# Optimization experiments

Hardware: AMD Instinct MI355X
Metric: run time of the kernel (lower is better)

Reference implementation:

```python
import jax, jax.numpy as jnp
import numpy as np

N_NODES = 50000
HIDDEN = 128
N_EDGES = 800000


def gcn_conv(x, edge_index, W, b):
    # PyG GCNConv: h = x @ W (no bias); add self-loops; symmetric norm; scatter-add; + bias
    h = x @ W  # [N, H]
    row, col = edge_index[0], edge_index[1]
    sl = jnp.arange(N_NODES)
    row_f = jnp.concatenate([row, sl])
    col_f = jnp.concatenate([col, sl])
    ones = jnp.ones(row_f.shape[0], dtype=x.dtype)
    deg = jax.ops.segment_sum(ones, col_f, num_segments=N_NODES)  # in-degree incl self-loop
    dinv = jnp.where(deg > 0, jax.lax.rsqrt(deg), 0.0)
    norm = dinv[row_f] * dinv[col_f]  # [E+N]
    msgs = h[row_f] * norm[:, None]   # gather + scale
    out = jax.ops.segment_sum(msgs, col_f, num_segments=N_NODES)  # scatter-add
    return out + b


def setup_inputs() -> dict:
    key = jax.random.key(0)
    ks = jax.random.split(key, 12)
    H = HIDDEN
    s = 1.0 / np.sqrt(H)
    x = jax.random.normal(ks[0], (N_NODES, H), dtype=jnp.float32)
    edge_index = jax.random.randint(ks[1], (2, N_EDGES), 0, N_NODES, dtype=jnp.int64)
    W1 = jax.random.uniform(ks[2], (H, H), jnp.float32, -s, s)
    b1 = jax.random.uniform(ks[3], (H,), jnp.float32, -s, s)
    W2 = jax.random.uniform(ks[4], (H, H), jnp.float32, -s, s)
    b2 = jax.random.uniform(ks[5], (H,), jnp.float32, -s, s)
    s2 = 1.0 / np.sqrt(2 * H)
    We1 = jax.random.uniform(ks[6], (2 * H, H), jnp.float32, -s2, s2)
    be1 = jax.random.uniform(ks[7], (H,), jnp.float32, -s2, s2)
    We2 = jax.random.uniform(ks[8], (H, 1), jnp.float32, -s, s)
    be2 = jax.random.uniform(ks[9], (1,), jnp.float32, -s, s)
    return {"x": x, "edge_index": edge_index, "W1": W1, "b1": b1, "W2": W2,
            "b2": b2, "We1": We1, "be1": be1, "We2": We2, "be2": be2}


def reference(x, edge_index, W1, b1, W2, b2, We1, be1, We2, be2):
    h = jax.nn.relu(gcn_conv(x, edge_index, W1, b1))
    h = jax.nn.relu(gcn_conv(h, edge_index, W2, b2))
    row, col = edge_index[0], edge_index[1]
    ef = jnp.concatenate([h[row], h[col]], axis=1)  # [E, 2H]
    z = jax.nn.relu(ef @ We1 + be1)
    p = jax.nn.sigmoid(z @ We2 + be2)  # [E, 1]
    return p.squeeze(-1)
```

## Files before the change

### kernel.cpp

```cpp
#include <hip/hip_runtime.h>
#include <math.h>

#define NND 50000
#define HD  128
#define NE  800000
#define NBK 196
#define BINB 391
#define NCH 391

typedef unsigned short u16;
typedef unsigned int   u32;
typedef __attribute__((ext_vector_type(8))) short bf16x8;
typedef __attribute__((ext_vector_type(4))) float f32x4;

__device__ __forceinline__ float bf2f(u32 u) {
  union { u32 i; float f; } v; v.i = u << 16; return v.f;
}
__device__ __forceinline__ u16 f2bf(float f) {
  union { float f; u32 i; } v; v.f = f;
  return (u16)((v.i + 0x7FFFu + ((v.i >> 16) & 1u)) >> 16);
}
__device__ __forceinline__ void unpack8(uint4 m, float* f) {
  f[0] = bf2f(m.x & 0xFFFFu); f[1] = bf2f(m.x >> 16);
  f[2] = bf2f(m.y & 0xFFFFu); f[3] = bf2f(m.y >> 16);
  f[4] = bf2f(m.z & 0xFFFFu); f[5] = bf2f(m.z >> 16);
  f[6] = bf2f(m.w & 0xFFFFu); f[7] = bf2f(m.w >> 16);
}

__global__ __launch_bounds__(256) void k_prep(const int* __restrict__ col, u32* __restrict__ bhist,
                                              const float* __restrict__ W1, const float* __restrict__ W2,
                                              const float* __restrict__ We1,
                                              u16* __restrict__ t1h, u16* __restrict__ t1l,
                                              u16* __restrict__ t2h, u16* __restrict__ t2l,
                                              u16* __restrict__ teh, u16* __restrict__ tel) {
  __shared__ u32 lh[NBK];
  int tid = threadIdx.x;
  if (blockIdx.x < BINB) {
    if (tid < NBK) lh[tid] = 0;
    __syncthreads();
    int e0 = blockIdx.x * 2048;
    #pragma unroll
    for (int s = 0; s < 8; ++s) {
      int e = e0 + s * 256 + tid;
      if (e < NE) atomicAdd(&lh[col[e] >> 8], 1u);
    }
    __syncthreads();
    if (tid < NBK && lh[tid]) atomicAdd(&bhist[tid], lh[tid]);
    return;
  }
  int idx = (blockIdx.x - BINB) * 256 + tid;
  float w;
  u16 *dh, *dl;
  int j;
  if (idx < 16384) {
    j = idx; int n = j >> 7, k = j & 127;
    w = W1[k * 128 + n]; dh = t1h; dl = t1l;
  } else if (idx < 32768) {
    j = idx - 16384; int n = j >> 7, k = j & 127;
    w = W2[k * 128 + n]; dh = t2h; dl = t2l;
  } else {
    j = idx - 32768; int n = j >> 7, k = j & 127;
    w = (n < 128) ? We1[k * 128 + n] : We1[(128 + k) * 128 + (n - 128)];
    dh = teh; dl = tel;
  }
  int n = j >> 7, k = j & 127;
  int sidx = n * 128 + ((((k >> 3) ^ (n & 7))) << 3) + (k & 7);
  u16 hi = f2bf(w);
  float res = w - bf2f((u32)hi);
  dh[sidx] = hi;
  dl[sidx] = f2bf(res);
}

__global__ __launch_bounds__(256) void k_bscan(const u32* __restrict__ bhist, u32* __restrict__ bbase,
                                               u32* __restrict__ bcur) {
  __shared__ u32 ws[4];
  int tid = threadIdx.x, lane = tid & 63, wid = tid >> 6;
  u32 d = (tid < NBK) ? bhist[tid] : 0;
  u32 x = d;
  #pragma unroll
  for (int off = 1; off < 64; off <<= 1) {
    u32 y = __shfl_up(x, off);
    if (lane >= off) x += y;
  }
  if (lane == 63) ws[wid] = x;
  __syncthreads();
  u32 woff = 0;
  for (int w = 0; w < wid; ++w) woff += ws[w];
  if (tid < NBK) { bbase[tid] = woff + x - d; bcur[tid] = woff + x - d; }
}

__global__ __launch_bounds__(256) void k_bin(const int* __restrict__ row, const int* __restrict__ col,
                                             u32* __restrict__ bcur, uint2* __restrict__ recs) {
  __shared__ u32 lcount[NBK], lbase[NBK];
  int tid = threadIdx.x;
  if (tid < NBK) lcount[tid] = 0;
  __syncthreads();
  int e0 = blockIdx.x * 2048;
  u32 rank[8]; int cv[8];
  #pragma unroll
  for (int s = 0; s < 8; ++s) {
    int e = e0 + s * 256 + tid;
    if (e < NE) {
      cv[s] = col[e];
      rank[s] = atomicAdd(&lcount[cv[s] >> 8], 1u);
    }
  }
  __syncthreads();
  if (tid < NBK && lcount[tid]) lbase[tid] = atomicAdd(&bcur[tid], lcount[tid]);
  __syncthreads();
  #pragma unroll
  for (int s = 0; s < 8; ++s) {
    int e = e0 + s * 256 + tid;
    if (e < NE) {
      int c = cv[s];
      u32 slot = lbase[c >> 8] + rank[s];
      recs[slot] = make_uint2((u32)row[e] | (((u32)c & 255u) << 16), (u32)e);
    }
  }
}

__global__ __launch_bounds__(256) void k_fine(const u32* __restrict__ bhist, const u32* __restrict__ bbase,
                                              const uint2* __restrict__ recs, uint2* __restrict__ sre,
                                              int* __restrict__ ptr, float* __restrict__ dinv) {
  __shared__ u32 lh[256];
  __shared__ u32 ws[4];
  int b = blockIdx.x, tid = threadIdx.x, lane = tid & 63, wid = tid >> 6;
  u32 base = bbase[b], cnt = bhist[b];
  lh[tid] = 0;
  __syncthreads();
  for (u32 i = tid; i < cnt; i += 256) atomicAdd(&lh[(recs[base + i].x >> 16) & 255u], 1u);
  __syncthreads();
  u32 ci = lh[tid];
  u32 x = ci;
  #pragma unroll
  for (int off = 1; off < 64; off <<= 1) {
    u32 y = __shfl_up(x, off);
    if (lane >= off) x += y;
  }
  if (lane == 63) ws[wid] = x;
  __syncthreads();
  u32 woff = 0;
  for (int w = 0; w < wid; ++w) woff += ws[w];
  u32 excl = woff + x - ci;
  int node = b * 256 + tid;
  if (node <= NND) ptr[node] = (int)(base + excl);
  if (node < NND) dinv[node] = rsqrtf((float)(ci + 1));
  __syncthreads();
  lh[tid] = excl;
  __syncthreads();
  for (u32 i = tid; i < cnt; i += 256) {
    uint2 rec = recs[base + i];
    u32 r = atomicAdd(&lh[(rec.x >> 16) & 255u], 1u);
    sre[base + r] = make_uint2(rec.x & 0xFFFFu, rec.y);
  }
}

__device__ __forceinline__ void mm_body(const void* Xv, bool afp32,
                                        const u16* Whi, const u16* Wlo,
                                        u16* OUT, const float* scale, int ostride,
                                        const float* bias) {
  __shared__ __align__(16) u16 Bh[128 * 128];
  __shared__ __align__(16) u16 Bl[128 * 128];
  int tid = threadIdx.x;
  int h = blockIdx.x / NCH;
  int chunk = blockIdx.x - h * NCH;
  Whi += (size_t)h * 128 * 128;
  Wlo += (size_t)h * 128 * 128;
  int ooff = h * 128;
  {
    const uint4* gh = (const uint4*)Whi;
    const uint4* gl = (const uint4*)Wlo;
    uint4* lh = (uint4*)Bh;
    uint4* ll = (uint4*)Bl;
    #pragma unroll
    for (int i = 0; i < 4; ++i) {
      lh[tid + i * 512] = gh[tid + i * 512];
      ll[tid + i * 512] = gl[tid + i * 512];
    }
  }
  __syncthreads();
  int wid = tid >> 6, lane = tid & 63;
  int m16 = lane & 15, kg = lane >> 4;
  int arow = chunk * 128 + wid * 16 + m16;
  int ar = (arow < NND) ? arow : NND - 1;
  bf16x8 afrag[4];
  if (afp32) {
    const float* X = (const float*)Xv + (size_t)ar * 128 + kg * 8;
    #pragma unroll
    for (int ks = 0; ks < 4; ++ks) {
      float4 a = *(const float4*)(X + ks * 32);
      float4 b = *(const float4*)(X + ks * 32 + 4);
      union { u32 w[4]; bf16x8 v; } u;
      u.w[0] = (u32)f2bf(a.x) | ((u32)f2bf(a.y) << 16);
      u.w[1] = (u32)f2bf(a.z) | ((u32)f2bf(a.w) << 16);
      u.w[2] = (u32)f2bf(b.x) | ((u32)f2bf(b.y) << 16);
      u.w[3] = (u32)f2bf(b.z) | ((u32)f2bf(b.w) << 16);
      afrag[ks] = u.v;
    }
  } else {
    const u16* X = (const u16*)Xv + (size_t)ar * 128 + kg * 8;
    #pragma unroll
    for (int ks = 0; ks < 4; ++ks) afrag[ks] = *(const bf16x8*)(X + ks * 32);
  }
  int crow0 = chunk * 128 + wid * 16 + kg * 4;
  float sc[4];
  #pragma unroll
  for (int j = 0; j < 4; ++j)
    sc[j] = (scale != nullptr && crow0 + j < NND) ? scale[crow0 + j] : 1.0f;
  #pragma unroll
  for (int t = 0; t < 8; ++t) {
    int coln = t * 16 + m16;
    float badd = (bias != nullptr && h != 0) ? bias[coln] : 0.f;
    f32x4 acc = {0.f, 0.f, 0.f, 0.f};
    #pragma unroll
    for (int ks = 0; ks < 4; ++ks) {
      int c8 = (ks * 4 + kg) ^ (coln & 7);
      bf16x8 bhf = *(const bf16x8*)(Bh + coln * 128 + c8 * 8);
      bf16x8 blf = *(const bf16x8*)(Bl + coln * 128 + c8 * 8);
      acc = __builtin_amdgcn_mfma_f32_16x16x32_bf16(afrag[ks], bhf, acc, 0, 0, 0);
      acc = __builtin_amdgcn_mfma_f32_16x16x32_bf16(afrag[ks], blf, acc, 0, 0, 0);
    }
    #pragma unroll
    for (int j = 0; j < 4; ++j) {
      int r = crow0 + j;
      if (r < NND) OUT[(size_t)r * ostride + ooff + coln] = f2bf(acc[j] * sc[j] + badd);
    }
  }
}

template<bool AFP32>
__global__ __launch_bounds__(512) void k_mm(const void* __restrict__ Xv,
                                            const u16* __restrict__ Whi, const u16* __restrict__ Wlo,
                                            u16* __restrict__ OUT, const float* __restrict__ scale,
                                            int ostride, const float* __restrict__ bias) {
  mm_body(Xv, AFP32, Whi, Wlo, OUT, scale, ostride, bias);
}

__global__ __launch_bounds__(256) void k_gather(const int* __restrict__ ptr, const uint2* __restrict__ sre,
                                                const float* __restrict__ dinv, const u16* __restrict__ Ts,
                                                u16* __restrict__ H, const float* __restrict__ bias) {
  int wid = threadIdx.x >> 6, lane = threadIdx.x & 63;
  int ch8 = lane & 15, slot = lane >> 4;
  int v = blockIdx.x * 4 + wid; if (v >= NND) return;
  int p0 = ptr[v], p1 = ptr[v + 1];
  const uint4* T4 = (const uint4*)Ts;
  float acc[8];
  if (slot == 0) {
    uint4 m = T4[(size_t)v * 16 + ch8];
    unpack8(m, acc);
  } else {
    #pragma unroll
    for (int k = 0; k < 8; ++k) acc[k] = 0.f;
  }
  for (int j2 = p0; j2 < p1; j2 += 32) {
    bool ok[8]; int r[8];
    #pragma unroll
    for (int u = 0; u < 8; ++u) {
      int j = j2 + u * 4 + slot;
      ok[u] = j < p1;
      r[u] = (int)sre[ok[u] ? j : p0].x;
    }
    uint4 m[8];
    #pragma unroll
    for (int u = 0; u < 8; ++u) m[u] = T4[(size_t)r[u] * 16 + ch8];
    #pragma unroll
    for (int u = 0; u < 8; ++u) {
      if (ok[u]) {
        float f[8]; unpack8(m[u], f);
        #pragma unroll
        for (int k = 0; k < 8; ++k) acc[k] += f[k];
      }
    }
  }
  #pragma unroll
  for (int k = 0; k < 8; ++k) {
    acc[k] += __shfl_xor(acc[k], 16);
    acc[k] += __shfl_xor(acc[k], 32);
  }
  if (slot == 0) {
    float s = dinv[v];
    float4 ba = *(const float4*)(bias + ch8 * 8);
    float4 bb = *(const float4*)(bias + ch8 * 8 + 4);
    float bv[8] = {ba.x, ba.y, ba.z, ba.w, bb.x, bb.y, bb.z, bb.w};
    u32 pk[4];
    #pragma unroll
    for (int k = 0; k < 4; ++k) {
      float o0 = fmaxf(fmaf(acc[2 * k], s, bv[2 * k]), 0.f);
      float o1 = fmaxf(fmaf(acc[2 * k + 1], s, bv[2 * k + 1]), 0.f);
      pk[k] = (u32)f2bf(o0) | ((u32)f2bf(o1) << 16);
    }
    *(uint4*)(H + (size_t)v * 128 + ch8 * 8) = make_uint4(pk[0], pk[1], pk[2], pk[3]);
  }
}

__global__ __launch_bounds__(256) void k_edge(const int* __restrict__ ptr, const uint2* __restrict__ sre,
                                              const u16* __restrict__ UV,
                                              const float* __restrict__ We2,
                                              const float* __restrict__ be2, float* __restrict__ out) {
  int wid = threadIdx.x >> 6, lane = threadIdx.x & 63;
  int ch8 = lane & 15, slot = lane >> 4;
  int c = blockIdx.x * 4 + wid; if (c >= NND) return;
  int p0 = ptr[c], p1 = ptr[c + 1];
  if (p0 == p1) return;
  const uint4* UV4 = (const uint4*)UV;
  float vv[8];
  {
    uint4 mv = UV4[(size_t)c * 32 + 16 + ch8];
    unpack8(mv, vv);
  }
  float w2[8];
  {
    float4 wa = *(const float4*)(We2 + ch8 * 8);
    float4 wb = *(const float4*)(We2 + ch8 * 8 + 4);
    w2[0] = wa.x; w2[1] = wa.y; w2[2] = wa.z; w2[3] = wa.w;
    w2[4] = wb.x; w2[5] = wb.y; w2[6] = wb.z; w2[7] = wb.w;
  }
  float bias2 = be2[0];
  for (int j2 = p0; j2 < p1; j2 += 32) {
    bool ok[8]; uint2 e[8];
    #pragma unroll
    for (int u = 0; u < 8; ++u) {
      int j = j2 + u * 4 + slot;
      ok[u] = j < p1;
      e[u] = sre[ok[u] ? j : p0];
    }
    uint4 m[8];
    #pragma unroll
    for (int u = 0; u < 8; ++u) m[u] = UV4[(size_t)e[u].x * 32 + ch8];
    float p[8];
    #pragma unroll
    for (int u = 0; u < 8; ++u) {
      float f[8]; unpack8(m[u], f);
      float s0 = fmaxf(f[0] + vv[0], 0.f) * w2[0] + fmaxf(f[1] + vv[1], 0.f) * w2[1];
      s0 += fmaxf(f[2] + vv[2], 0.f) * w2[2] + fmaxf(f[3] + vv[3], 0.f) * w2[3];
      s0 += fmaxf(f[4] + vv[4], 0.f) * w2[4] + fmaxf(f[5] + vv[5], 0.f) * w2[5];
      s0 += fmaxf(f[6] + vv[6], 0.f) * w2[6] + fmaxf(f[7] + vv[7], 0.f) * w2[7];
      p[u] = s0;
    }
    #pragma unroll
    for (int off = 8; off; off >>= 1) {
      #pragma unroll
      for (int u = 0; u < 8; ++u) p[u] += __shfl_xor(p[u], off);
    }
    if (ch8 == 0) {
      #pragma unroll
      for (int u = 0; u < 8; ++u)
        if (ok[u]) out[e[u].y] = 1.f / (1.f + __expf(-(p[u] + bias2)));
    }
  }
}

extern "C" void kernel_launch(void* const* d_in, const int* in_sizes, int n_in,
                              void* d_out, int out_size, void* d_ws, size_t ws_size,
                              hipStream_t stream) {
  const float* x   = (const float*)d_in[0];
  const int*   ei  = (const int*)d_in[1];
  const float* W1  = (const float*)d_in[2];
  const float* b1  = (const float*)d_in[3];
  const float* W2  = (const float*)d_in[4];
  const float* b2  = (const float*)d_in[5];
  const float* We1 = (const float*)d_in[6];
  const float* be1 = (const float*)d_in[7];
  const float* We2 = (const float*)d_in[8];
  const float* be2 = (const float*)d_in[9];
  float* out = (float*)d_out;

  const int* row  = ei;
  const int* colp = ei + NE;

  if (ws_size < (size_t)16166240 * 4) return;
  int*   ptr    = (int*)d_ws;
  float* dinv   = (float*)d_ws + 50064;
  u32*   bhist  = (u32*)d_ws + 100112;
  u32*   bbase  = (u32*)d_ws + 100308;
  u32*   bcur   = (u32*)d_ws + 100504;
  uint2* recs   = (uint2*)((u32*)d_ws + 100704);
  uint2* sre    = (uint2*)((u32*)d_ws + 1700704);
  u16*   t1h    = (u16*)((u32*)d_ws + 3300704);
  u16*   t1l    = (u16*)((u32*)d_ws + 3308896);
  u16*   t2h    = (u16*)((u32*)d_ws + 3317088);
  u16*   t2l    = (u16*)((u32*)d_ws + 3325280);
  u16*   teh    = (u16*)((u32*)d_ws + 3333472);
  u16*   tel    = (u16*)((u32*)d_ws + 3349856);
  u16*   Ts     = (u16*)((u32*)d_ws + 3366240);
  u16*   H      = (u16*)((u32*)d_ws + 6566240);
  u16*   UV     = (u16*)((u32*)d_ws + 9766240);

  (void)hipMemsetAsync(bhist, 0, NBK * sizeof(u32), stream);
  k_prep <<<BINB + 256, 256, 0, stream>>>(colp, bhist, W1, W2, We1, t1h, t1l, t2h, t2l, teh, tel);
  k_bscan<<<1, 256, 0, stream>>>(bhist, bbase, bcur);
  k_bin  <<<BINB, 256, 0, stream>>>(row, colp, bcur, recs);
  k_fine <<<NBK, 256, 0, stream>>>(bhist, bbase, recs, sre, ptr, dinv);

  int node_grid = (NND + 3) / 4;

  k_mm<true><<<NCH, 512, 0, stream>>>(x, t1h, t1l, Ts, dinv, 128, nullptr);
  k_gather<<<node_grid, 256, 0, stream>>>(ptr, sre, dinv, Ts, H, b1);

  k_mm<false><<<NCH, 512, 0, stream>>>(H, t2h, t2l, Ts, dinv, 128, nullptr);
  k_gather<<<node_grid, 256, 0, stream>>>(ptr, sre, dinv, Ts, H, b2);

  k_mm<false><<<2 * NCH, 512, 0, stream>>>(H, teh, tel, UV, nullptr, 256, be1);
  k_edge<<<node_grid, 256, 0, stream>>>(ptr, sre, UV, We2, be2, out);
}
```

Before: 206.0 us.

## Re-sort edges by source range and make edge scoring edge-parallel

Adds a stable counting sort (histogram, scan, place) that groups the column-sorted edge list into 8 buckets by source-node range, and packs the destination node into the upper bits of each record. The final edge kernel now gives each wave a fixed run of 32 edges instead of one destination node. It reloads the destination's V vector only when the destination changes, and gathers U rows from a narrower source range so they are more likely to stay in cache. This removes per-node load imbalance and improves gather locality, at the cost of three extra small kernels and another edge-array pass.

```diff
diff --git a/kernel.cpp b/kernel.cpp
--- a/kernel.cpp
+++ b/kernel.cpp
@@ -7,9 +7,13 @@
 #define NBK 196
 #define BINB 391
 #define NCH 391
+#define RB  8
+#define RBSZ 6250
+#define RBLK 391
 
 typedef unsigned short u16;
 typedef unsigned int   u32;
+typedef unsigned long long u64;
 typedef __attribute__((ext_vector_type(8))) short bf16x8;
 typedef __attribute__((ext_vector_type(4))) float f32x4;
 
@@ -150,8 +154,105 @@
   __syncthreads();
   for (u32 i = tid; i < cnt; i += 256) {
     uint2 rec = recs[base + i];
-    u32 r = atomicAdd(&lh[(rec.x >> 16) & 255u], 1u);
-    sre[base + r] = make_uint2(rec.x & 0xFFFFu, rec.y);
+    u32 cidx = (rec.x >> 16) & 255u;
+    u32 r = atomicAdd(&lh[cidx], 1u);
+    sre[base + r] = make_uint2((rec.x & 0xFFFFu) | (((u32)b * 256u + cidx) << 16), rec.y);
+  }
+}
+
+__global__ __launch_bounds__(256) void k_rhist(const uint2* __restrict__ sre, u32* __restrict__ rcnt) {
+  __shared__ u32 lc[RB];
+  int tid = threadIdx.x, lane = tid & 63, wid = tid >> 6;
+  if (tid < RB) lc[tid] = 0;
+  __syncthreads();
+  int e0 = blockIdx.x * 2048;
+  #pragma unroll
+  for (int s = 0; s < 8; ++s) {
+    int e = e0 + s * 256 + wid * 64 + lane;
+    int rb = -1;
+    if (e < NE) rb = (int)((sre[e].x & 0xFFFFu) / RBSZ);
+    #pragma unroll
+    for (int b = 0; b < RB; ++b) {
+      u64 m = __ballot(rb == b);
+      if (lane == 0 && m) atomicAdd(&lc[b], (u32)__popcll(m));
+    }
+  }
+  __syncthreads();
+  if (tid < RB) rcnt[blockIdx.x * RB + tid] = lc[tid];
+}
+
+__global__ __launch_bounds__(256) void k_rscan(const u32* __restrict__ rcnt, u32* __restrict__ roff) {
+  __shared__ u32 ws[4];
+  __shared__ u32 carry;
+  int tid = threadIdx.x, lane = tid & 63, wid = tid >> 6;
+  if (tid == 0) carry = 0;
+  __syncthreads();
+  for (int base = 0; base < RB * RBLK + 255; base += 256) {
+    int i = base + tid;
+    u32 d = 0;
+    if (i < RB * RBLK) { int b = i / RBLK, blk = i - b * RBLK; d = rcnt[blk * RB + b]; }
+    u32 x = d;
+    #pragma unroll
+    for (int off = 1; off < 64; off <<= 1) {
+      u32 y = __shfl_up(x, off);
+      if (lane >= off) x += y;
+    }
+    if (lane == 63) ws[wid] = x;
+    __syncthreads();
+    u32 woff = 0;
+    for (int w = 0; w < wid; ++w) woff += ws[w];
+    if (i < RB * RBLK) { int b = i / RBLK, blk = i - b * RBLK; roff[blk * RB + b] = carry + woff + x - d; }
+    __syncthreads();
+    if (tid == 255) carry += woff + x;
+    __syncthreads();
+  }
+}
+
+__global__ __launch_bounds__(256) void k_rplace(const uint2* __restrict__ sre, const u32* __restrict__ roff,
+                                                uint2* __restrict__ sre2) {
+  __shared__ u32 scnt[32][RB];
+  __shared__ u32 sexc[32][RB];
+  __shared__ u32 sbase[RB];
+  int tid = threadIdx.x, lane = tid & 63, wid = tid >> 6;
+  if (tid < RB) sbase[tid] = roff[blockIdx.x * RB + tid];
+  int e0 = blockIdx.x * 2048;
+  u32 rank[8]; int rbv[8]; uint2 rec[8];
+  #pragma unroll
+  for (int s = 0; s < 8; ++s) {
+    int e = e0 + s * 256 + wid * 64 + lane;
+    int rb = -1;
+    uint2 r = make_uint2(0u, 0u);
+    if (e < NE) { r = sre[e]; rb = (int)((r.x & 0xFFFFu) / RBSZ); }
+    rec[s] = r; rbv[s] = rb;
+    u32 rk = 0;
+    #pragma unroll
+    for (int b = 0; b < RB; ++b) {
+      u64 m = __ballot(rb == b);
+      if (rb == b) rk = (u32)__popcll(m & ((1ull << lane) - 1ull));
+      if (lane == 0) scnt[s * 4 + wid][b] = (u32)__popcll(m);
+    }
+    rank[s] = rk;
+  }
+  __syncthreads();
+  {
+    int b = tid >> 5, slot = tid & 31;
+    u32 d = scnt[slot][b];
+    u32 x = d;
+    #pragma unroll
+    for (int off = 1; off < 32; off <<= 1) {
+      u32 y = __shfl_up(x, off, 32);
+      if (slot >= off) x += y;
+    }
+    sexc[slot][b] = x - d;
+  }
+  __syncthreads();
+  #pragma unroll
+  for (int s = 0; s < 8; ++s) {
+    if (rbv[s] >= 0) {
+      int slot = s * 4 + wid;
+      u32 dst = sbase[rbv[s]] + sexc[slot][rbv[s]] + rank[s];
+      sre2[dst] = rec[s];
+    }
   }
 }
 
@@ -258,7 +359,7 @@
     for (int u = 0; u < 8; ++u) {
       int j = j2 + u * 4 + slot;
       ok[u] = j < p1;
-      r[u] = (int)sre[ok[u] ? j : p0].x;
+      r[u] = (int)(sre[ok[u] ? j : p0].x & 0xFFFFu);
     }
     uint4 m[8];
     #pragma unroll
@@ -293,21 +394,14 @@
   }
 }
 
-__global__ __launch_bounds__(256) void k_edge(const int* __restrict__ ptr, const uint2* __restrict__ sre,
+__global__ __launch_bounds__(256) void k_edge(const uint2* __restrict__ sre2,
                                               const u16* __restrict__ UV,
                                               const float* __restrict__ We2,
                                               const float* __restrict__ be2, float* __restrict__ out) {
   int wid = threadIdx.x >> 6, lane = threadIdx.x & 63;
   int ch8 = lane & 15, slot = lane >> 4;
-  int c = blockIdx.x * 4 + wid; if (c >= NND) return;
-  int p0 = ptr[c], p1 = ptr[c + 1];
-  if (p0 == p1) return;
+  int e0 = (blockIdx.x * 4 + wid) * 32 + slot * 8;
   const uint4* UV4 = (const uint4*)UV;
-  float vv[8];
-  {
-    uint4 mv = UV4[(size_t)c * 32 + 16 + ch8];
-    unpack8(mv, vv);
-  }
   float w2[8];
   {
     float4 wa = *(const float4*)(We2 + ch8 * 8);
@@ -316,37 +410,39 @@
     w2[4] = wb.x; w2[5] = wb.y; w2[6] = wb.z; w2[7] = wb.w;
   }
   float bias2 = be2[0];
-  for (int j2 = p0; j2 < p1; j2 += 32) {
-    bool ok[8]; uint2 e[8];
-    #pragma unroll
-    for (int u = 0; u < 8; ++u) {
-      int j = j2 + u * 4 + slot;
-      ok[u] = j < p1;
-      e[u] = sre[ok[u] ? j : p0];
-    }
-    uint4 m[8];
-    #pragma unroll
-    for (int u = 0; u < 8; ++u) m[u] = UV4[(size_t)e[u].x * 32 + ch8];
-    float p[8];
-    #pragma unroll
-    for (int u = 0; u < 8; ++u) {
-      float f[8]; unpack8(m[u], f);
-      float s0 = fmaxf(f[0] + vv[0], 0.f) * w2[0] + fmaxf(f[1] + vv[1], 0.f) * w2[1];
-      s0 += fmaxf(f[2] + vv[2], 0.f) * w2[2] + fmaxf(f[3] + vv[3], 0.f) * w2[3];
-      s0 += fmaxf(f[4] + vv[4], 0.f) * w2[4] + fmaxf(f[5] + vv[5], 0.f) * w2[5];
-      s0 += fmaxf(f[6] + vv[6], 0.f) * w2[6] + fmaxf(f[7] + vv[7], 0.f) * w2[7];
-      p[u] = s0;
-    }
-    #pragma unroll
-    for (int off = 8; off; off >>= 1) {
-      #pragma unroll
-      for (int u = 0; u < 8; ++u) p[u] += __shfl_xor(p[u], off);
-    }
-    if (ch8 == 0) {
-      #pragma unroll
-      for (int u = 0; u < 8; ++u)
-        if (ok[u]) out[e[u].y] = 1.f / (1.f + __expf(-(p[u] + bias2)));
-    }
+  uint2 e[8];
+  #pragma unroll
+  for (int u = 0; u < 8; ++u) e[u] = sre2[e0 + u];
+  uint4 m[8];
+  #pragma unroll
+  for (int u = 0; u < 8; ++u) m[u] = UV4[(size_t)(e[u].x & 0xFFFFu) * 32 + ch8];
+  float p[8];
+  float vv[8];
+  u32 ccur = 0xFFFFFFFFu;
+  #pragma unroll
+  for (int u = 0; u < 8; ++u) {
+    u32 c = e[u].x >> 16;
+    if (c != ccur) {
+      uint4 mv = UV4[(size_t)c * 32 + 16 + ch8];
+      unpack8(mv, vv);
+      ccur = c;
+    }
+    float f[8]; unpack8(m[u], f);
+    float s0 = fmaxf(f[0] + vv[0], 0.f) * w2[0] + fmaxf(f[1] + vv[1], 0.f) * w2[1];
+    s0 += fmaxf(f[2] + vv[2], 0.f) * w2[2] + fmaxf(f[3] + vv[3], 0.f) * w2[3];
+    s0 += fmaxf(f[4] + vv[4], 0.f) * w2[4] + fmaxf(f[5] + vv[5], 0.f) * w2[5];
+    s0 += fmaxf(f[6] + vv[6], 0.f) * w2[6] + fmaxf(f[7] + vv[7], 0.f) * w2[7];
+    p[u] = s0;
+  }
+  #pragma unroll
+  for (int off = 8; off; off >>= 1) {
+    #pragma unroll
+    for (int u = 0; u < 8; ++u) p[u] += __shfl_xor(p[u], off);
+  }
+  if (ch8 == 0) {
+    #pragma unroll
+    for (int u = 0; u < 8; ++u)
+      out[e[u].y] = 1.f / (1.f + __expf(-(p[u] + bias2)));
   }
 }
 
@@ -368,31 +464,38 @@
   const int* row  = ei;
   const int* colp = ei + NE;
 
-  if (ws_size < (size_t)16166240 * 4) return;
+  if (ws_size < (size_t)17772640 * 4) return;
   int*   ptr    = (int*)d_ws;
   float* dinv   = (float*)d_ws + 50064;
   u32*   bhist  = (u32*)d_ws + 100112;
   u32*   bbase  = (u32*)d_ws + 100308;
   u32*   bcur   = (u32*)d_ws + 100504;
-  uint2* recs   = (uint2*)((u32*)d_ws + 100704);
-  uint2* sre    = (uint2*)((u32*)d_ws + 1700704);
-  u16*   t1h    = (u16*)((u32*)d_ws + 3300704);
-  u16*   t1l    = (u16*)((u32*)d_ws + 3308896);
-  u16*   t2h    = (u16*)((u32*)d_ws + 3317088);
-  u16*   t2l    = (u16*)((u32*)d_ws + 3325280);
-  u16*   teh    = (u16*)((u32*)d_ws + 3333472);
-  u16*   tel    = (u16*)((u32*)d_ws + 3349856);
-  u16*   Ts     = (u16*)((u32*)d_ws + 3366240);
-  u16*   H      = (u16*)((u32*)d_ws + 6566240);
-  u16*   UV     = (u16*)((u32*)d_ws + 9766240);
+  u32*   rcnt   = (u32*)d_ws + 100704;
+  u32*   roff   = (u32*)d_ws + 103904;
+  uint2* recs   = (uint2*)((u32*)d_ws + 107104);
+  uint2* sre    = (uint2*)((u32*)d_ws + 1707104);
+  uint2* sre2   = (uint2*)((u32*)d_ws + 3307104);
+  u16*   t1h    = (u16*)((u32*)d_ws + 4907104);
+  u16*   t1l    = (u16*)((u32*)d_ws + 4915296);
+  u16*   t2h    = (u16*)((u32*)d_ws + 4923488);
+  u16*   t2l    = (u16*)((u32*)d_ws + 4931680);
+  u16*   teh    = (u16*)((u32*)d_ws + 4939872);
+  u16*   tel    = (u16*)((u32*)d_ws + 4956256);
+  u16*   Ts     = (u16*)((u32*)d_ws + 4972640);
+  u16*   H      = (u16*)((u32*)d_ws + 8172640);
+  u16*   UV     = (u16*)((u32*)d_ws + 11372640);
 
   (void)hipMemsetAsync(bhist, 0, NBK * sizeof(u32), stream);
-  k_prep <<<BINB + 256, 256, 0, stream>>>(colp, bhist, W1, W2, We1, t1h, t1l, t2h, t2l, teh, tel);
-  k_bscan<<<1, 256, 0, stream>>>(bhist, bbase, bcur);
-  k_bin  <<<BINB, 256, 0, stream>>>(row, colp, bcur, recs);
-  k_fine <<<NBK, 256, 0, stream>>>(bhist, bbase, recs, sre, ptr, dinv);
+  k_prep  <<<BINB + 256, 256, 0, stream>>>(colp, bhist, W1, W2, We1, t1h, t1l, t2h, t2l, teh, tel);
+  k_bscan <<<1, 256, 0, stream>>>(bhist, bbase, bcur);
+  k_bin   <<<BINB, 256, 0, stream>>>(row, colp, bcur, recs);
+  k_fine  <<<NBK, 256, 0, stream>>>(bhist, bbase, recs, sre, ptr, dinv);
+  k_rhist <<<RBLK, 256, 0, stream>>>(sre, rcnt);
+  k_rscan <<<1, 256, 0, stream>>>(rcnt, roff);
+  k_rplace<<<RBLK, 256, 0, stream>>>(sre, roff, sre2);
 
   int node_grid = (NND + 3) / 4;
+  int edge_grid = NE / 128;
 
   k_mm<true><<<NCH, 512, 0, stream>>>(x, t1h, t1l, Ts, dinv, 128, nullptr);
   k_gather<<<node_grid, 256, 0, stream>>>(ptr, sre, dinv, Ts, H, b1);
@@ -401,5 +504,5 @@
   k_gather<<<node_grid, 256, 0, stream>>>(ptr, sre, dinv, Ts, H, b2);
 
   k_mm<false><<<2 * NCH, 512, 0, stream>>>(H, teh, tel, UV, nullptr, 256, be1);
-  k_edge<<<node_grid, 256, 0, stream>>>(ptr, sre, UV, We2, be2, out);
-}
+  k_edge<<<edge_grid, 256, 0, stream>>>(sre2, UV, We2, be2, out);
+}
```

After: 235.6 us. 1.14x slower.
